# Kernel optimization log

Measured on AMD Instinct MI355X. Metric: run time of the kernel, lower is better.

The kernel has to match this reference:

```python
import jax, jax.numpy as jnp
import numpy as np

NUM_HEADS = 8


def setup_inputs() -> dict:
    key = jax.random.key(0)
    ks = jax.random.split(key, 9)
    B, C, H, W = 2, 64, 48, 48
    Ck, Cv, Co = 64, 64, 64
    s = lambda fan_in: 1.0 / np.sqrt(fan_in)
    return {
        "x": jax.random.normal(ks[0], (B, C, H, W), jnp.float32),
        "Wq": jax.random.normal(ks[1], (Ck, C), jnp.float32) * s(C),
        "bq": jnp.zeros((Ck,), jnp.float32),
        "Wk": jax.random.normal(ks[2], (Ck, C), jnp.float32) * s(C),
        "bk": jnp.zeros((Ck,), jnp.float32),
        "Wv": jax.random.normal(ks[3], (Cv, C), jnp.float32) * s(C),
        "bv": jnp.zeros((Cv,), jnp.float32),
        "Wo": jax.random.normal(ks[4], (Co, Cv), jnp.float32) * s(Cv),
        "bo": jnp.zeros((Co,), jnp.float32),
    }


def _conv1x1(x, W, b):
    # 1x1 conv == channel matmul: [B,C,H,W] x [O,C] -> [B,O,H,W]
    return jnp.einsum("oc,bchw->bohw", W, x) + b[None, :, None, None]


def reference(x, Wq, bq, Wk, bk, Wv, bv, Wo, bo):
    B, _, H, W_ = x.shape
    nh = NUM_HEADS
    Ck, Cv = Wq.shape[0], Wv.shape[0]
    d = Ck // nh
    L = H * W_

    # NOTE: original torch code scales q in place via a view, so returned q is scaled.
    q = _conv1x1(x, Wq, bq) * (d ** -0.5)
    k = _conv1x1(x, Wk, bk)
    v = _conv1x1(x, Wv, bv)

    qs = q.reshape(B, nh, d, L)          # [B,h,d,Lq]
    ks = k.reshape(B, nh, d, L)          # [B,h,d,Lk]
    vs = v.reshape(B, nh, Cv // nh, L)   # [B,h,dv,Lk]

    logits = jnp.einsum("bhdq,bhdk->bhqk", qs, ks)   # [B,h,Lq,Lk]
    # softmax over the QUERY axis (dim=2), as in the original nn.Softmax(dim=2)
    weights = jax.nn.softmax(logits, axis=2)
    o = jnp.einsum("bhck,bhqk->bhcq", vs, weights)   # [B,h,dv,Lq]

    o = o.reshape(B, Cv, H, W_)
    out = _conv1x1(o, Wo, bo)
    return out, q
```

## Files before the change

### kernel.cpp

```cpp
#include <hip/hip_runtime.h>

#define LL   2304
#define CCH  64
#define NHD  8

static constexpr float QSCALE = 0.35355339059327373f;
static constexpr float LOG2E  = 1.4426950408889634f;

typedef _Float16 half2_t  __attribute__((ext_vector_type(2)));
typedef _Float16 half4_t  __attribute__((ext_vector_type(4)));
typedef _Float16 half8_t  __attribute__((ext_vector_type(8)));
typedef float    float16_t __attribute__((ext_vector_type(16)));

__device__ __forceinline__ half2_t pk_f16(float a, float b) {
    return __builtin_bit_cast(half2_t, __builtin_amdgcn_cvt_pkrtz(a, b));
}


__global__ __launch_bounds__(256) void k_qkv(
    const float* __restrict__ x,
    const float* __restrict__ Wq, const float* __restrict__ bq,
    const float* __restrict__ Wk, const float* __restrict__ bk,
    const float* __restrict__ Wv, const float* __restrict__ bv,
    float* __restrict__ qout,
    _Float16* __restrict__ Qt, _Float16* __restrict__ Kt, _Float16* __restrict__ Vt)
{
    __shared__ float xs[64][32];
    __shared__ float wsm[64][64];
    const int t   = threadIdx.x;
    const int l0  = blockIdx.x * 32;
    const int b   = blockIdx.y;
    const int mat = blockIdx.z;
    const float* W    = (mat == 0) ? Wq : (mat == 1 ? Wk : Wv);
    const float* bias = (mat == 0) ? bq : (mat == 1 ? bk : bv);
    const float* xb = x + (long)b * CCH * LL;

    #pragma unroll
    for (int p = 0; p < 2; ++p) {
        int flat = (p * 256 + t) * 4;
        int c = flat >> 5, l = flat & 31;
        *(float4*)&xs[c][l] = *(const float4*)&xb[(long)c * LL + l0 + l];
    }
    #pragma unroll
    for (int p = 0; p < 4; ++p) {
        int flat = (p * 256 + t) * 4;
        int c = flat >> 6, l = flat & 63;
        *(float4*)&wsm[c][l] = *(const float4*)&W[flat];
    }
    __syncthreads();

    const int l  = t & 31;
    const int cg = t >> 5;
    float acc[8];
    #pragma unroll
    for (int j = 0; j < 8; ++j) acc[j] = 0.f;
    for (int cp = 0; cp < 64; ++cp) {
        float xv = xs[cp][l];
        #pragma unroll
        for (int j = 0; j < 8; ++j) acc[j] = fmaf(wsm[cg * 8 + j][cp], xv, acc[j]);
    }
    long row = (long)(b * NHD + cg) * LL + l0 + l;
    if (mat == 0) {
        half8_t pq;
        #pragma unroll
        for (int j = 0; j < 8; ++j) {
            float qv = (acc[j] + bias[cg * 8 + j]) * QSCALE;
            qout[((long)b * CCH + cg * 8 + j) * LL + l0 + l] = qv;
            pq[j] = (_Float16)(qv * LOG2E);
        }
        *(half8_t*)(Qt + row * 8) = pq;
    } else if (mat == 1) {
        half8_t pk;
        #pragma unroll
        for (int j = 0; j < 8; ++j) pk[j] = (_Float16)(acc[j] + bias[cg * 8 + j]);
        *(half8_t*)(Kt + row * 8) = pk;
    } else {
        half8_t pv;
        #pragma unroll
        for (int j = 0; j < 8; ++j) pv[j] = (_Float16)(acc[j] + bias[cg * 8 + j]);
        *(half8_t*)(Vt + row * 8) = pv;
    }
}

__global__ __launch_bounds__(256) void k_denom(
    const _Float16* __restrict__ Qt, const _Float16* __restrict__ Kt,
    const _Float16* __restrict__ Vt, _Float16* __restrict__ V2)
{
    __shared__ _Float16 lQ[2][256][4];
    __shared__ float Dp[4][32];
    __shared__ float rDs[32];
    const int t    = threadIdx.x;
    const int bh   = blockIdx.y;
    const int k0   = blockIdx.x * 32;
    const int lane = t & 63, w = t >> 6;
    const int half = lane >> 5, l31 = lane & 31;

    half4_t kA = *(const half4_t*)(Kt + ((long)bh * LL + k0 + l31) * 8 + half * 4);

    const float4* qbase = (const float4*)(Qt + (long)bh * LL * 8);
    float4 pre = qbase[t];

    float16_t Dacc = {};
    for (int ch = 0; ch < 9; ++ch) {
        __syncthreads();
        *(float2*)&lQ[0][t][0] = make_float2(pre.x, pre.y);
        *(float2*)&lQ[1][t][0] = make_float2(pre.z, pre.w);
        __syncthreads();
        if (ch + 1 < 9) pre = qbase[(ch + 1) * 256 + t];
        #pragma unroll
        for (int T = 0; T < 2; ++T) {
            half4_t qB = *(const half4_t*)&lQ[half][(2 * w + T) * 32 + l31][0];
            float16_t S = __builtin_amdgcn_mfma_f32_32x32x8f16(kA, qB, (float16_t){}, 0, 0, 0);
            #pragma unroll
            for (int r = 0; r < 16; ++r) Dacc[r] += __builtin_amdgcn_exp2f(S[r]);
        }
    }
    #pragma unroll
    for (int r = 0; r < 16; ++r) {
        float v = Dacc[r];
        v += __shfl_xor(v, 1);  v += __shfl_xor(v, 2);  v += __shfl_xor(v, 4);
        v += __shfl_xor(v, 8);  v += __shfl_xor(v, 16);
        Dacc[r] = v;
    }
    if (l31 == 0) {
        #pragma unroll
        for (int r = 0; r < 16; ++r) {
            int row = (r & 3) + 8 * (r >> 2) + 4 * half;
            Dp[w][row] = Dacc[r];
        }
    }
    __syncthreads();
    if (t < 32) rDs[t] = 256.0f / (Dp[0][t] + Dp[1][t] + Dp[2][t] + Dp[3][t]);
    __syncthreads();
    {
        int kk = t >> 3, c = t & 7;
        float v = (float)Vt[((long)bh * LL + k0 + kk) * 8 + c];
        V2[((long)bh * 8 + c) * LL + k0 + kk] = (_Float16)(v * rDs[kk]);
    }
}

__global__ __launch_bounds__(256) void k_av(
    const _Float16* __restrict__ Qt, const _Float16* __restrict__ Kt,
    const _Float16* __restrict__ V2, float* __restrict__ ot)
{
    __shared__ _Float16 lK[2][64][4];
    __shared__ _Float16 lVt[8][72];
    const int t    = threadIdx.x;
    const int bh   = blockIdx.y;
    const int s    = blockIdx.z;
    const int b = bh >> 3, h = bh & 7;
    const int lane = t & 63, w = t >> 6;
    const int half = lane >> 5, l31 = lane & 31;
    const int q0   = blockIdx.x * 128 + w * 32;

    half4_t qB = *(const half4_t*)(Qt + ((long)bh * LL + q0 + l31) * 8 + half * 4);

    const long ks0 = (long)s * 576;
    const float4*    kbase = (const float4*)(Kt + ((long)bh * LL + ks0) * 8);
    const _Float16*  vbase = V2 + (long)bh * 8 * LL + ks0;

    float4 preK, preV;
    if (t < 64) preK = kbase[t];
    else if (t < 128) {
        int c = (t - 64) >> 3, j8 = (t - 64) & 7;
        preV = *(const float4*)(vbase + (long)c * LL + j8 * 8);
    }

    float16_t O = {};
    for (int ch = 0; ch < 9; ++ch) {
        __syncthreads();
        if (t < 64) {
            *(float2*)&lK[0][t][0] = make_float2(preK.x, preK.y);
            *(float2*)&lK[1][t][0] = make_float2(preK.z, preK.w);
        } else if (t < 128) {
            int c = (t - 64) >> 3, j8 = (t - 64) & 7;
            *(float4*)&lVt[c][j8 * 8] = preV;
        }
        __syncthreads();
        if (ch + 1 < 9) {
            if (t < 64) preK = kbase[(ch + 1) * 64 + t];
            else if (t < 128) {
                int c = (t - 64) >> 3, j8 = (t - 64) & 7;
                preV = *(const float4*)(vbase + (long)c * LL + (ch + 1) * 64 + j8 * 8);
            }
        }
        const int cl = l31 & 7;
        #pragma unroll
        for (int T = 0; T < 2; ++T) {
            int kb = T * 32;
            half4_t kA = *(const half4_t*)&lK[half][kb + l31][0];
            float16_t S = __builtin_amdgcn_mfma_f32_32x32x8f16(kA, qB, (float16_t){}, 0, 0, 0);
            #pragma unroll
            for (int g = 0; g < 4; ++g) {
                half2_t p0 = pk_f16(__builtin_amdgcn_exp2f(S[4 * g + 0]),
                                    __builtin_amdgcn_exp2f(S[4 * g + 1]));
                half2_t p1 = pk_f16(__builtin_amdgcn_exp2f(S[4 * g + 2]),
                                    __builtin_amdgcn_exp2f(S[4 * g + 3]));
                half4_t pB = __builtin_shufflevector(p0, p1, 0, 1, 2, 3);
                half4_t vA = *(const half4_t*)&lVt[cl][kb + g * 8 + half * 4];
                O = __builtin_amdgcn_mfma_f32_32x32x8f16(vA, pB, O, 0, 0, 0);
            }
        }
    }
    float* otb = ot + (long)s * (2 * CCH * LL) + ((long)b * CCH + h * 8) * LL;
    #pragma unroll
    for (int r = 0; r < 4; ++r) {
        int c = r + 4 * half;
        otb[(long)c * LL + q0 + l31] = O[r] * (1.0f / 256.0f);
    }
}

__global__ __launch_bounds__(256) void k_out(
    const float* __restrict__ ot, const float* __restrict__ Wo,
    const float* __restrict__ bo, float* __restrict__ out)
{
    __shared__ float os[64][32];
    __shared__ float wsm[64][64];
    const int t  = threadIdx.x;
    const int l0 = blockIdx.x * 32;
    const int b  = blockIdx.y;
    const long SLAB = 2 * CCH * (long)LL;
    const float* ob = ot + (long)b * CCH * LL;

    #pragma unroll
    for (int p = 0; p < 2; ++p) {
        int flat = (p * 256 + t) * 4;
        int cv = flat >> 5, l = flat & 31;
        long off = (long)cv * LL + l0 + l;
        float4 a = *(const float4*)&ob[off];
        #pragma unroll
        for (int s = 1; s < 4; ++s) {
            float4 bb = *(const float4*)&ob[s * SLAB + off];
            a.x += bb.x; a.y += bb.y; a.z += bb.z; a.w += bb.w;
        }
        *(float4*)&os[cv][l] = a;
    }
    #pragma unroll
    for (int p = 0; p < 4; ++p) {
        int flat = (p * 256 + t) * 4;
        int c = flat >> 6, l = flat & 63;
        *(float4*)&wsm[c][l] = *(const float4*)&Wo[flat];
    }
    __syncthreads();

    const int l  = t & 31;
    const int cg = t >> 5;
    float acc[8];
    #pragma unroll
    for (int j = 0; j < 8; ++j) acc[j] = 0.f;
    for (int cv = 0; cv < 64; ++cv) {
        float xv = os[cv][l];
        #pragma unroll
        for (int j = 0; j < 8; ++j) acc[j] = fmaf(wsm[cg * 8 + j][cv], xv, acc[j]);
    }
    #pragma unroll
    for (int j = 0; j < 8; ++j) {
        int co = cg * 8 + j;
        out[((long)b * CCH + co) * LL + l0 + l] = acc[j] + bo[co];
    }
}

extern "C" void kernel_launch(void* const* d_in, const int* in_sizes, int n_in,
                              void* d_out, int out_size, void* d_ws, size_t ws_size,
                              hipStream_t stream)
{
    const float* x  = (const float*)d_in[0];
    const float* Wq = (const float*)d_in[1];
    const float* bq = (const float*)d_in[2];
    const float* Wk = (const float*)d_in[3];
    const float* bk = (const float*)d_in[4];
    const float* Wv = (const float*)d_in[5];
    const float* bv = (const float*)d_in[6];
    const float* Wo = (const float*)d_in[7];
    const float* bo = (const float*)d_in[8];

    float* out  = (float*)d_out;
    float* qout = out + 294912;

    _Float16* Qt = (_Float16*)d_ws;
    _Float16* Kt = Qt + 294912;
    _Float16* Vt = Kt + 294912;
    _Float16* V2 = Vt + 294912;
    float*    ot = (float*)(V2 + 294912);

    k_qkv  <<<dim3(72, 2, 3),  256, 0, stream>>>(x, Wq, bq, Wk, bk, Wv, bv, qout, Qt, Kt, Vt);
    k_denom<<<dim3(72, 16),    256, 0, stream>>>(Qt, Kt, Vt, V2);
    k_av   <<<dim3(18, 16, 4), 256, 0, stream>>>(Qt, Kt, V2, ot);
    k_out  <<<dim3(72, 2),     256, 0, stream>>>(ot, Wo, bo, out);
}
```

Measured before the change: 110.0 us.

## Fuse output projection into attention kernel via atomic accumulation

Removes the separate k_out kernel and the fp32 split-K partial buffer. Each attention block now applies its head's slice of Wo to its 8-channel output tile and atomically adds the result into the final output. The output is pre-initialised with the bias inside k_qkv. This saves one launch and a round trip of the partial slabs through memory, but adds many global float atomics (64 channels per query per split per head), a per-block transposed-Wo LDS fill, more register pressure, and non-deterministic summation order.

```diff
diff --git a/kernel.cpp b/kernel.cpp
--- a/kernel.cpp
+++ b/kernel.cpp
@@ -22,7 +22,8 @@
     const float* __restrict__ Wq, const float* __restrict__ bq,
     const float* __restrict__ Wk, const float* __restrict__ bk,
     const float* __restrict__ Wv, const float* __restrict__ bv,
-    float* __restrict__ qout,
+    const float* __restrict__ bo,
+    float* __restrict__ qout, float* __restrict__ outp,
     _Float16* __restrict__ Qt, _Float16* __restrict__ Kt, _Float16* __restrict__ Vt)
 {
     __shared__ float xs[64][32];
@@ -35,6 +36,17 @@
     const float* bias = (mat == 0) ? bq : (mat == 1 ? bk : bv);
     const float* xb = x + (long)b * CCH * LL;
 
+    if (mat == 0) {
+        #pragma unroll
+        for (int p = 0; p < 2; ++p) {
+            int flat = (p * 256 + t) * 4;
+            int co = flat >> 5, l = flat & 31;
+            float bv4 = bo[co];
+            float4 vv = make_float4(bv4, bv4, bv4, bv4);
+            *(float4*)&outp[((long)b * CCH + co) * LL + l0 + l] = vv;
+        }
+    }
+
     #pragma unroll
     for (int p = 0; p < 2; ++p) {
         int flat = (p * 256 + t) * 4;
@@ -139,12 +151,14 @@
     }
 }
 
-__global__ __launch_bounds__(256) void k_av(
+__global__ __launch_bounds__(256, 4) void k_av_out(
     const _Float16* __restrict__ Qt, const _Float16* __restrict__ Kt,
-    const _Float16* __restrict__ V2, float* __restrict__ ot)
+    const _Float16* __restrict__ V2, const float* __restrict__ Wo,
+    float* __restrict__ out)
 {
     __shared__ _Float16 lK[2][64][4];
     __shared__ _Float16 lVt[8][72];
+    __shared__ float WoT[64][68];
     const int t    = threadIdx.x;
     const int bh   = blockIdx.y;
     const int s    = blockIdx.z;
@@ -152,6 +166,15 @@
     const int lane = t & 63, w = t >> 6;
     const int half = lane >> 5, l31 = lane & 31;
     const int q0   = blockIdx.x * 128 + w * 32;
+
+    #pragma unroll
+    for (int p = 0; p < 4; ++p) {
+        int flat = p * 256 + t;
+        int co = flat >> 4, cv4 = flat & 15;
+        float4 v = *(const float4*)&Wo[co * 64 + cv4 * 4];
+        WoT[cv4 * 4 + 0][co] = v.x; WoT[cv4 * 4 + 1][co] = v.y;
+        WoT[cv4 * 4 + 2][co] = v.z; WoT[cv4 * 4 + 3][co] = v.w;
+    }
 
     half4_t qB = *(const half4_t*)(Qt + ((long)bh * LL + q0 + l31) * 8 + half * 4);
 
@@ -202,61 +225,37 @@
             }
         }
     }
-    float* otb = ot + (long)s * (2 * CCH * LL) + ((long)b * CCH + h * 8) * LL;
+
+    float ocl[4], och[4];
     #pragma unroll
     for (int r = 0; r < 4; ++r) {
-        int c = r + 4 * half;
-        otb[(long)c * LL + q0 + l31] = O[r] * (1.0f / 256.0f);
-    }
-}
-
-__global__ __launch_bounds__(256) void k_out(
-    const float* __restrict__ ot, const float* __restrict__ Wo,
-    const float* __restrict__ bo, float* __restrict__ out)
-{
-    __shared__ float os[64][32];
-    __shared__ float wsm[64][64];
-    const int t  = threadIdx.x;
-    const int l0 = blockIdx.x * 32;
-    const int b  = blockIdx.y;
-    const long SLAB = 2 * CCH * (long)LL;
-    const float* ob = ot + (long)b * CCH * LL;
-
-    #pragma unroll
-    for (int p = 0; p < 2; ++p) {
-        int flat = (p * 256 + t) * 4;
-        int cv = flat >> 5, l = flat & 31;
-        long off = (long)cv * LL + l0 + l;
-        float4 a = *(const float4*)&ob[off];
-        #pragma unroll
-        for (int s = 1; s < 4; ++s) {
-            float4 bb = *(const float4*)&ob[s * SLAB + off];
-            a.x += bb.x; a.y += bb.y; a.z += bb.z; a.w += bb.w;
-        }
-        *(float4*)&os[cv][l] = a;
-    }
-    #pragma unroll
-    for (int p = 0; p < 4; ++p) {
-        int flat = (p * 256 + t) * 4;
-        int c = flat >> 6, l = flat & 63;
-        *(float4*)&wsm[c][l] = *(const float4*)&Wo[flat];
-    }
-    __syncthreads();
-
-    const int l  = t & 31;
-    const int cg = t >> 5;
-    float acc[8];
-    #pragma unroll
-    for (int j = 0; j < 8; ++j) acc[j] = 0.f;
-    for (int cv = 0; cv < 64; ++cv) {
-        float xv = os[cv][l];
-        #pragma unroll
-        for (int j = 0; j < 8; ++j) acc[j] = fmaf(wsm[cg * 8 + j][cv], xv, acc[j]);
-    }
-    #pragma unroll
-    for (int j = 0; j < 8; ++j) {
-        int co = cg * 8 + j;
-        out[((long)b * CCH + co) * LL + l0 + l] = acc[j] + bo[co];
+        float mine  = O[r] * (1.0f / 256.0f);
+        float other = __shfl_xor(mine, 32);
+        ocl[r] = half ? other : mine;
+        och[r] = half ? mine  : other;
+    }
+    float* ob = out + ((long)b * CCH) * LL + q0 + l31;
+    #pragma unroll
+    for (int g = 0; g < 2; ++g) {
+        const int co0 = half * 32 + g * 16;
+        float acc2[16];
+        #pragma unroll
+        for (int j = 0; j < 16; ++j) acc2[j] = 0.f;
+        #pragma unroll
+        for (int c = 0; c < 8; ++c) {
+            float ov = (c < 4) ? ocl[c] : och[c - 4];
+            #pragma unroll
+            for (int j4 = 0; j4 < 4; ++j4) {
+                const float4 wv = *(const float4*)&WoT[h * 8 + c][co0 + j4 * 4];
+                acc2[j4 * 4 + 0] = fmaf(wv.x, ov, acc2[j4 * 4 + 0]);
+                acc2[j4 * 4 + 1] = fmaf(wv.y, ov, acc2[j4 * 4 + 1]);
+                acc2[j4 * 4 + 2] = fmaf(wv.z, ov, acc2[j4 * 4 + 2]);
+                acc2[j4 * 4 + 3] = fmaf(wv.w, ov, acc2[j4 * 4 + 3]);
+            }
+        }
+        #pragma unroll
+        for (int j = 0; j < 16; ++j)
+            atomicAdd(ob + (long)(co0 + j) * LL, acc2[j]);
     }
 }
 
@@ -281,10 +280,9 @@
     _Float16* Kt = Qt + 294912;
     _Float16* Vt = Kt + 294912;
     _Float16* V2 = Vt + 294912;
-    float*    ot = (float*)(V2 + 294912);
-
-    k_qkv  <<<dim3(72, 2, 3),  256, 0, stream>>>(x, Wq, bq, Wk, bk, Wv, bv, qout, Qt, Kt, Vt);
-    k_denom<<<dim3(72, 16),    256, 0, stream>>>(Qt, Kt, Vt, V2);
-    k_av   <<<dim3(18, 16, 4), 256, 0, stream>>>(Qt, Kt, V2, ot);
-    k_out  <<<dim3(72, 2),     256, 0, stream>>>(ot, Wo, bo, out);
-}
+
+    k_qkv   <<<dim3(72, 2, 3),  256, 0, stream>>>(x, Wq, bq, Wk, bk, Wv, bv, bo,
+                                                  qout, out, Qt, Kt, Vt);
+    k_denom <<<dim3(72, 16),    256, 0, stream>>>(Qt, Kt, Vt, V2);
+    k_av_out<<<dim3(18, 16, 4), 256, 0, stream>>>(Qt, Kt, V2, Wo, out);
+}
```

Measured after the change: 127.3 us. +15.8%, slower.
